# Optimization experiments

Measured on AMD Instinct MI355X. Metric: run time of the kernel, lower is better.

## Reference

```python
import jax, jax.numpy as jnp
import numpy as np

N, E = 20000, 160000
D_NODE_IN, D_EDGE_IN = 256, 64
D = 128          # node/edge feature dim
H = 256          # edge hidden dim
T = 17           # number of keypoint types
EDGE_STEPS, NODE_STEPS = 2, 1


def _w(k, shape):
    return jax.random.normal(k, shape, dtype=jnp.float32) / np.sqrt(shape[-2] if len(shape) > 1 else shape[-1]).astype(np.float32)


def setup_inputs() -> dict:
    key = jax.random.key(0)
    ks = iter(jax.random.split(key, 40))
    inp = {
        'x': jax.random.normal(next(ks), (N, D_NODE_IN), dtype=jnp.float32),
        'edge_attr': jax.random.normal(next(ks), (E, D_EDGE_IN), dtype=jnp.float32),
        'edge_index': jax.random.randint(next(ks), (2, E), 0, N),
        'node_types': jax.random.randint(next(ks), (N,), 0, T),
        # type-routed node embedding: 17 stacked 2-layer MLPs 256->128->128
        'ne_w1': _w(next(ks), (T, D_NODE_IN, D)), 'ne_b1': jnp.zeros((T, D)),
        'ne_w2': _w(next(ks), (T, D, D)),         'ne_b2': jnp.zeros((T, D)),
        # edge embedding 64->128->128
        'ee_w1': _w(next(ks), (D_EDGE_IN, D)), 'ee_b1': jnp.zeros((D,)),
        'ee_w2': _w(next(ks), (D, D)),         'ee_b2': jnp.zeros((D,)),
        # MPLayer edge MLP: [x_i, x_j, e] with skip -> (2*2D + 2D)=768 -> 256 -> 128
        'me_w1': _w(next(ks), (4 * D + 2 * D, H)), 'me_b1': jnp.zeros((H,)),
        'me_w2': _w(next(ks), (H, D)),             'me_b2': jnp.zeros((D,)),
        # MPLayer node update: [x(skip 2D), agg(D)] -> 128
        'mn_w1': _w(next(ks), (2 * D + D, D)), 'mn_b1': jnp.zeros((D,)),
        # classifiers
        'ec_w1': _w(next(ks), (D, D)), 'ec_b1': jnp.zeros((D,)),
        'ec_w2': _w(next(ks), (D, 1)), 'ec_b2': jnp.zeros((1,)),
        'nc_w1': _w(next(ks), (D, D)), 'nc_b1': jnp.zeros((D,)),
        'nc_w2': _w(next(ks), (D, 1)), 'nc_b2': jnp.zeros((1,)),
        'cc_w1': _w(next(ks), (D, D)), 'cc_b1': jnp.zeros((D,)),
        'cc_w2': _w(next(ks), (D, T)), 'cc_b2': jnp.zeros((T,)),
    }
    return inp


def _mlp2(x, w1, b1, w2, b2):
    return jax.nn.relu(x @ w1 + b1) @ w2 + b2


def reference(x, edge_attr, edge_index, node_types,
              ne_w1, ne_b1, ne_w2, ne_b2,
              ee_w1, ee_b1, ee_w2, ee_b2,
              me_w1, me_b1, me_w2, me_b2,
              mn_w1, mn_b1,
              ec_w1, ec_b1, ec_w2, ec_b2,
              nc_w1, nc_b1, nc_w2, nc_b2,
              cc_w1, cc_b1, cc_w2, cc_b2):
    n = x.shape[0]
    # NodeMlpType: run all 17 MLPs, select by node type (same math as masked dispatch)
    h = jax.nn.relu(jnp.einsum('nd,tdk->tnk', x, ne_w1) + ne_b1[:, None, :])   # [T,N,D]
    o = jnp.einsum('tnk,tkm->tnm', h, ne_w2) + ne_b2[:, None, :]               # [T,N,D]
    nf0 = o[node_types, jnp.arange(n)]                                          # [N,D]
    ef0 = _mlp2(edge_attr, ee_w1, ee_b1, ee_w2, ee_b2)                          # [E,D]

    src, dst = edge_index[0], edge_index[1]

    def mp_step(nf, ef):
        nf_c = jnp.concatenate([nf0, nf], axis=1)                               # skip concat [N,2D]
        ef_c = jnp.concatenate([ef0, ef], axis=1)                               # [E,2D]
        m = jnp.concatenate([nf_c[dst], nf_c[src], ef_c], axis=1)               # [E,6D]
        e_new = _mlp2(m, me_w1, me_b1, me_w2, me_b2)                            # [E,D]
        agg = jax.ops.segment_sum(e_new, dst, num_segments=n)                   # aggr='add'
        nf_new = jnp.concatenate([nf_c, agg], axis=1) @ mn_w1 + mn_b1           # [N,D]
        return nf_new, e_new

    nf, ef = nf0, ef0
    for _ in range(EDGE_STEPS):
        nf, ef = mp_step(nf, ef)
    pred_edge = _mlp2(ef, ec_w1, ec_b1, ec_w2, ec_b2).squeeze(-1)               # [E]
    for _ in range(NODE_STEPS):
        nf, ef = mp_step(nf, ef)
    pred_node = _mlp2(nf, nc_w1, nc_b1, nc_w2, nc_b2).squeeze(-1)               # [N]
    pred_class = _mlp2(nf, cc_w1, cc_b1, cc_w2, cc_b2)                          # [N,T]
    return (pred_edge, pred_node, pred_class, nf, ef)
```

## Files before the change

### kernel.cpp

```cpp
#include <hip/hip_runtime.h>
#include <hip/hip_bf16.h>

#define N_NODES 20000
#define N_EDGES 160000
#define DIN_NODE 256
#define DIN_EDGE 64
#define DF 128
#define HH 256
#define TT 17
#define NE_PAD_SLOTS 20544
#define NB_NODE (NE_PAD_SLOTS / 32)

typedef __attribute__((ext_vector_type(8))) short short8v;
typedef __attribute__((ext_vector_type(4))) float f32x4;

__device__ __forceinline__ unsigned short f2bf(float f) {
  unsigned int u = __builtin_bit_cast(unsigned int, f);
  u += 0x7FFFu + ((u >> 16) & 1u);
  return (unsigned short)(u >> 16);
}

__device__ __forceinline__ float bf2f(unsigned short u) {
  return __builtin_bit_cast(float, (unsigned int)u << 16);
}

__device__ __forceinline__ short8v pack8(float4 a, float4 b) {
  short8v o;
  o[0] = (short)f2bf(a.x); o[1] = (short)f2bf(a.y);
  o[2] = (short)f2bf(a.z); o[3] = (short)f2bf(a.w);
  o[4] = (short)f2bf(b.x); o[5] = (short)f2bf(b.y);
  o[6] = (short)f2bf(b.z); o[7] = (short)f2bf(b.w);
  return o;
}

struct PackPtrs {
  const float *s0, *s1, *s2, *s3, *s4, *s5, *s6, *s7, *s8, *s9, *s10, *s11;
  unsigned short *d0, *d1, *d2, *d3, *d4, *d5, *d6, *d7, *d8, *d9, *d10, *d11;
};

__global__ __launch_bounds__(256) void k_pack_all(PackPtrs P) {
  const int g = blockIdx.x * 4 + (threadIdx.x >> 6);
  const int l = threadIdx.x & 63;
  if (g >= 2320) return;
  const float* w; unsigned short* out; int K, N, tile;
  if (g < 128)       { w = P.s0;  out = P.d0;  K = 256; N = 256; tile = g; }
  else if (g < 256)  { w = P.s1;  out = P.d1;  K = 256; N = 256; tile = g - 128; }
  else if (g < 384)  { w = P.s2;  out = P.d2;  K = 256; N = 256; tile = g - 256; }
  else if (g < 448)  { w = P.s3;  out = P.d3;  K = 256; N = 128; tile = g - 384; }
  else if (g < 544)  { w = P.s4;  out = P.d4;  K = 384; N = 128; tile = g - 448; }
  else if (g < 1632) { w = P.s5;  out = P.d5;  K = 256; N = 128; tile = g - 544; }
  else if (g < 2176) { w = P.s6;  out = P.d6;  K = 128; N = 128; tile = g - 1632; }
  else if (g < 2192) { w = P.s7;  out = P.d7;  K = 64;  N = 128; tile = g - 2176; }
  else if (g < 2224) { w = P.s8;  out = P.d8;  K = 128; N = 128; tile = g - 2192; }
  else if (g < 2256) { w = P.s9;  out = P.d9;  K = 128; N = 128; tile = g - 2224; }
  else if (g < 2288) { w = P.s10; out = P.d10; K = 128; N = 128; tile = g - 2256; }
  else               { w = P.s11; out = P.d11; K = 128; N = 128; tile = g - 2288; }
  const int ntTiles = N >> 4;
  const int tilesPer = (K >> 5) * ntTiles;
  const int bt = tile / tilesPer;
  const int rr = tile - bt * tilesPer;
  const int kt = rr / ntTiles, nt = rr - kt * ntTiles;
  const float* wb = w + (size_t)bt * K * N;
  const int col = (nt << 4) + (l & 15);
  const int k0 = (kt << 5) + ((l >> 4) << 3);
  unsigned short* o = out + (((size_t)tile << 6) + l) * 8;
#pragma unroll
  for (int j = 0; j < 8; ++j) o[j] = f2bf(wb[(size_t)(k0 + j) * N + col]);
}

__global__ void k_count_deg(const int* __restrict__ types,
                            const int* __restrict__ dstv,
                            int* __restrict__ cnt, int* __restrict__ deg) {
  const int i = blockIdx.x * 256 + threadIdx.x;
  if (i < N_NODES) atomicAdd(&cnt[types[i]], 1);
  if (i < N_EDGES) atomicAdd(&deg[dstv[i]], 1);
}

__global__ __launch_bounds__(256) void k_prefix_scan(
    const int* __restrict__ cnt, int* __restrict__ woff,
    const int* __restrict__ deg, int* __restrict__ rs, int* __restrict__ wo) {
  __shared__ int partial[256];
  const int t = threadIdx.x;
  if (t == 0) {
    int cur = 0;
    for (int ty = 0; ty < TT; ++ty) {
      woff[ty] = cur;
      cur += (cnt[ty] + 31) & ~31;
    }
  }
  const int base = t * 80;
  int s = 0;
  for (int j = 0; j < 80; ++j) {
    const int n = base + j;
    if (n < N_NODES) s += deg[n];
  }
  partial[t] = s;
  __syncthreads();
  for (int off = 1; off < 256; off <<= 1) {
    const int v = (t >= off) ? partial[t - off] : 0;
    __syncthreads();
    partial[t] += v;
    __syncthreads();
  }
  int run = (t > 0) ? partial[t - 1] : 0;
  for (int j = 0; j < 80; ++j) {
    const int n = base + j;
    if (n < N_NODES) {
      rs[n] = run; wo[n] = run;
      run += deg[n];
    }
  }
  if (t == 255) rs[N_NODES] = run;
}

__global__ void k_scatter_elist(const int* __restrict__ types,
                                const int* __restrict__ srcv,
                                const int* __restrict__ dstv,
                                int* __restrict__ woff, int* __restrict__ wo,
                                int* __restrict__ bucket,
                                int* __restrict__ elist, int* __restrict__ ipos,
                                int* __restrict__ srcp, int* __restrict__ dstp) {
  const int i = blockIdx.x * 256 + threadIdx.x;
  if (i < N_NODES) {
    const int pos = atomicAdd(&woff[types[i]], 1);
    bucket[pos] = i;
  }
  if (i < N_EDGES) {
    const int pos = atomicAdd(&wo[dstv[i]], 1);
    elist[pos] = i;
    ipos[i] = pos;
    srcp[pos] = srcv[i];
    dstp[pos] = dstv[i];
  }
}

__global__ __launch_bounds__(256) void k_embed_fused(
    const float* __restrict__ x, const int* __restrict__ bucket,
    const int* __restrict__ types,
    const unsigned short* __restrict__ wp1, const float* __restrict__ b1,
    const unsigned short* __restrict__ wp2, const float* __restrict__ b2,
    unsigned short* __restrict__ nf0b,
    const unsigned short* __restrict__ wpd, const unsigned short* __restrict__ wps,
    unsigned short* __restrict__ PDo, unsigned short* __restrict__ PSo,
    const float* __restrict__ ea, const int* __restrict__ ipos,
    const unsigned short* __restrict__ ewp1, const float* __restrict__ eb1,
    const unsigned short* __restrict__ ewp2, const float* __restrict__ eb2,
    unsigned short* __restrict__ ef0p) {
  __shared__ __align__(16) unsigned char A[32 * 512];
  __shared__ __align__(16) unsigned char Hb[32 * 256];
  __shared__ int sidx[32];
  const int t = threadIdx.x;
  const int w = t >> 6, l = t & 63, lr = l & 15, lg = l >> 4;
  const int sw = (lr & 7) << 4;
  const int row0 = lr, row1 = 16 + lr;

  if (blockIdx.x < NB_NODE) {
    const int r0 = blockIdx.x * 32;
    if (t < 32) sidx[t] = bucket[r0 + t];
    __syncthreads();
    if (sidx[0] < 0) return;
    const int ty = types[sidx[0]];

#pragma unroll
    for (int j = 0; j < 4; ++j) {
      const int q = j * 256 + t;
      const int i = q >> 5, c = q & 31;
      const int nd = sidx[i];
      short8v o;
      if (nd >= 0) {
        const float* xr = x + (size_t)nd * DIN_NODE + c * 8;
        o = pack8(*reinterpret_cast<const float4*>(xr),
                  *reinterpret_cast<const float4*>(xr + 4));
      } else {
#pragma unroll
        for (int k = 0; k < 8; ++k) o[k] = 0;
      }
      *reinterpret_cast<short8v*>(A + ((i * 512 + c * 16) ^ ((i & 7) << 4))) = o;
    }
    __syncthreads();

    f32x4 acc[2][2];
#pragma unroll
    for (int mt = 0; mt < 2; ++mt)
#pragma unroll
      for (int q = 0; q < 2; ++q)
#pragma unroll
        for (int r = 0; r < 4; ++r) acc[mt][q][r] = 0.f;
#pragma unroll
    for (int kt = 0; kt < 8; ++kt) {
      const short8v a0 = *reinterpret_cast<const short8v*>(
          A + ((row0 * 512 + kt * 64 + lg * 16) ^ sw));
      const short8v a1 = *reinterpret_cast<const short8v*>(
          A + ((row1 * 512 + kt * 64 + lg * 16) ^ sw));
#pragma unroll
      for (int q = 0; q < 2; ++q) {
        const short8v bq = *reinterpret_cast<const short8v*>(
            wp1 + (((size_t)(ty * 64 + kt * 8 + 2 * w + q) * 64 + l) << 3));
        acc[0][q] = __builtin_amdgcn_mfma_f32_16x16x32_bf16(a0, bq, acc[0][q], 0, 0, 0);
        acc[1][q] = __builtin_amdgcn_mfma_f32_16x16x32_bf16(a1, bq, acc[1][q], 0, 0, 0);
      }
    }
#pragma unroll
    for (int q = 0; q < 2; ++q) {
      const int col = (2 * w + q) * 16 + lr;
      const float bias = b1[ty * DF + col];
#pragma unroll
      for (int mt = 0; mt < 2; ++mt)
#pragma unroll
        for (int r = 0; r < 4; ++r) {
          const int row = mt * 16 + lg * 4 + r;
          *reinterpret_cast<unsigned short*>(
              Hb + ((row * 256 + col * 2) ^ ((row & 7) << 4))) =
              f2bf(fmaxf(acc[mt][q][r] + bias, 0.f));
        }
    }
    __syncthreads();

    f32x4 acc2[2][2];
#pragma unroll
    for (int mt = 0; mt < 2; ++mt)
#pragma unroll
      for (int q = 0; q < 2; ++q)
#pragma unroll
        for (int r = 0; r < 4; ++r) acc2[mt][q][r] = 0.f;
#pragma unroll
    for (int kt = 0; kt < 4; ++kt) {
      const short8v a0 = *reinterpret_cast<const short8v*>(
          Hb + ((row0 * 256 + kt * 64 + lg * 16) ^ sw));
      const short8v a1 = *reinterpret_cast<const short8v*>(
          Hb + ((row1 * 256 + kt * 64 + lg * 16) ^ sw));
#pragma unroll
      for (int q = 0; q < 2; ++q) {
        const short8v bq = *reinterpret_cast<const short8v*>(
            wp2 + (((size_t)(ty * 32 + kt * 8 + 2 * w + q) * 64 + l) << 3));
        acc2[0][q] = __builtin_amdgcn_mfma_f32_16x16x32_bf16(a0, bq, acc2[0][q], 0, 0, 0);
        acc2[1][q] = __builtin_amdgcn_mfma_f32_16x16x32_bf16(a1, bq, acc2[1][q], 0, 0, 0);
      }
    }
#pragma unroll
    for (int q = 0; q < 2; ++q) {
      const int col = (2 * w + q) * 16 + lr;
      const float bias = b2[ty * DF + col];
#pragma unroll
      for (int mt = 0; mt < 2; ++mt)
#pragma unroll
        for (int r = 0; r < 4; ++r) {
          const int row = mt * 16 + lg * 4 + r;
          const int nd = sidx[row];
          const unsigned short v = f2bf(acc2[mt][q][r] + bias);
          if (nd >= 0) nf0b[(size_t)nd * DF + col] = v;
          *reinterpret_cast<unsigned short*>(
              A + ((row * 512 + col * 2) ^ ((row & 7) << 4))) = v;
          *reinterpret_cast<unsigned short*>(
              A + ((row * 512 + (col + 128) * 2) ^ ((row & 7) << 4))) = v;
        }
    }
    __syncthreads();

    f32x4 aD[2][4], aS[2][4];
#pragma unroll
    for (int mt = 0; mt < 2; ++mt)
#pragma unroll
      for (int q = 0; q < 4; ++q)
#pragma unroll
        for (int r = 0; r < 4; ++r) { aD[mt][q][r] = 0.f; aS[mt][q][r] = 0.f; }
    const int r0o = lr * 512 + lg * 16, r1o = (16 + lr) * 512 + lg * 16;
#pragma unroll
    for (int kt = 0; kt < 8; ++kt) {
      const short8v a0 = *reinterpret_cast<const short8v*>(A + ((r0o + kt * 64) ^ sw));
      const short8v a1 = *reinterpret_cast<const short8v*>(A + ((r1o + kt * 64) ^ sw));
#pragma unroll
      for (int q = 0; q < 4; ++q) {
        const size_t bi = (((size_t)(kt * 16 + 4 * w + q) * 64 + l) << 3);
        const short8v bD = *reinterpret_cast<const short8v*>(wpd + bi);
        const short8v bS = *reinterpret_cast<const short8v*>(wps + bi);
        aD[0][q] = __builtin_amdgcn_mfma_f32_16x16x32_bf16(a0, bD, aD[0][q], 0, 0, 0);
        aD[1][q] = __builtin_amdgcn_mfma_f32_16x16x32_bf16(a1, bD, aD[1][q], 0, 0, 0);
        aS[0][q] = __builtin_amdgcn_mfma_f32_16x16x32_bf16(a0, bS, aS[0][q], 0, 0, 0);
        aS[1][q] = __builtin_amdgcn_mfma_f32_16x16x32_bf16(a1, bS, aS[1][q], 0, 0, 0);
      }
    }
#pragma unroll
    for (int q = 0; q < 4; ++q) {
      const int col = (4 * w + q) * 16 + lr;
#pragma unroll
      for (int mt = 0; mt < 2; ++mt)
#pragma unroll
        for (int r = 0; r < 4; ++r) {
          const int row = mt * 16 + lg * 4 + r;
          const int nd = sidx[row];
          if (nd >= 0) {
            PDo[(size_t)nd * HH + col] = f2bf(aD[mt][q][r]);
            PSo[(size_t)nd * HH + col] = f2bf(aS[mt][q][r]);
          }
        }
    }
  } else {
    const int e0 = (blockIdx.x - NB_NODE) * 32;
    if (t < 32) sidx[t] = ipos[e0 + t];
    {
      const int i = t >> 3, c = t & 7;
      const float* xr = ea + (size_t)(e0 + i) * DIN_EDGE + c * 8;
      const short8v o = pack8(*reinterpret_cast<const float4*>(xr),
                              *reinterpret_cast<const float4*>(xr + 4));
      *reinterpret_cast<short8v*>(A + ((i * 128 + c * 16) ^ ((i & 7) << 4))) = o;
    }
    __syncthreads();

    f32x4 acc[2][2];
#pragma unroll
    for (int mt = 0; mt < 2; ++mt)
#pragma unroll
      for (int q = 0; q < 2; ++q)
#pragma unroll
        for (int r = 0; r < 4; ++r) acc[mt][q][r] = 0.f;
#pragma unroll
    for (int kt = 0; kt < 2; ++kt) {
      const short8v a0 = *reinterpret_cast<const short8v*>(
          A + ((row0 * 128 + kt * 64 + lg * 16) ^ sw));
      const short8v a1 = *reinterpret_cast<const short8v*>(
          A + ((row1 * 128 + kt * 64 + lg * 16) ^ sw));
#pragma unroll
      for (int q = 0; q < 2; ++q) {
        const short8v bq = *reinterpret_cast<const short8v*>(
            ewp1 + (((size_t)(kt * 8 + 2 * w + q) * 64 + l) << 3));
        acc[0][q] = __builtin_amdgcn_mfma_f32_16x16x32_bf16(a0, bq, acc[0][q], 0, 0, 0);
        acc[1][q] = __builtin_amdgcn_mfma_f32_16x16x32_bf16(a1, bq, acc[1][q], 0, 0, 0);
      }
    }
#pragma unroll
    for (int q = 0; q < 2; ++q) {
      const int col = (2 * w + q) * 16 + lr;
      const float bias = eb1[col];
#pragma unroll
      for (int mt = 0; mt < 2; ++mt)
#pragma unroll
        for (int r = 0; r < 4; ++r) {
          const int row = mt * 16 + lg * 4 + r;
          *reinterpret_cast<unsigned short*>(
              Hb + ((row * 256 + col * 2) ^ ((row & 7) << 4))) =
              f2bf(fmaxf(acc[mt][q][r] + bias, 0.f));
        }
    }
    __syncthreads();

    f32x4 acc2[2][2];
#pragma unroll
    for (int mt = 0; mt < 2; ++mt)
#pragma unroll
      for (int q = 0; q < 2; ++q)
#pragma unroll
        for (int r = 0; r < 4; ++r) acc2[mt][q][r] = 0.f;
#pragma unroll
    for (int kt = 0; kt < 4; ++kt) {
      const short8v a0 = *reinterpret_cast<const short8v*>(
          Hb + ((row0 * 256 + kt * 64 + lg * 16) ^ sw));
      const short8v a1 = *reinterpret_cast<const short8v*>(
          Hb + ((row1 * 256 + kt * 64 + lg * 16) ^ sw));
#pragma unroll
      for (int q = 0; q < 2; ++q) {
        const short8v bq = *reinterpret_cast<const short8v*>(
            ewp2 + (((size_t)(kt * 8 + 2 * w + q) * 64 + l) << 3));
        acc2[0][q] = __builtin_amdgcn_mfma_f32_16x16x32_bf16(a0, bq, acc2[0][q], 0, 0, 0);
        acc2[1][q] = __builtin_amdgcn_mfma_f32_16x16x32_bf16(a1, bq, acc2[1][q], 0, 0, 0);
      }
    }
#pragma unroll
    for (int q = 0; q < 2; ++q) {
      const int col = (2 * w + q) * 16 + lr;
      const float bias = eb2[col];
#pragma unroll
      for (int mt = 0; mt < 2; ++mt)
#pragma unroll
        for (int r = 0; r < 4; ++r) {
          const int row = mt * 16 + lg * 4 + r;
          ef0p[(size_t)sidx[row] * DF + col] = f2bf(acc2[mt][q][r] + bias);
        }
    }
  }
}

template <bool OUTF, bool HEAD>
__global__ __launch_bounds__(256) void k_edge_mlp_mfma(
    const unsigned short* __restrict__ ef0, const unsigned short* __restrict__ ef_in,
    unsigned short* __restrict__ ef_out, float* __restrict__ ef_outf,
    const int* __restrict__ srcp, const int* __restrict__ dstp,
    const int* __restrict__ elist,
    const unsigned short* __restrict__ wpe, const float* __restrict__ b1,
    const unsigned short* __restrict__ wp2, const float* __restrict__ b2,
    const unsigned short* __restrict__ PDi, const unsigned short* __restrict__ PSi,
    const unsigned short* __restrict__ wech, const float* __restrict__ hb1,
    const float* __restrict__ hw2, const float* __restrict__ hb2,
    float* __restrict__ out_pe) {
  __shared__ __align__(16) unsigned char A_lds[32 * 512];
  __shared__ __align__(16) unsigned char P_lds[32 * 512];
  __shared__ int sd[2][32];
  __shared__ int se[32];
  __shared__ float hpart[32][8];
  const int t = threadIdx.x;
  const int e0 = blockIdx.x * 32;
  if (t < 32) sd[0][t] = srcp[e0 + t];
  else if (t < 64) sd[1][t - 32] = dstp[e0 + t - 32];
  else if ((OUTF || HEAD) && t < 96) se[t - 64] = elist[e0 + t - 64];

#pragma unroll
  for (int j = 0; j < 4; ++j) {
    const int q = j * 256 + t;
    const int i = q >> 5, c = q & 31;
    const unsigned short* bp = (c < 16)
        ? ef0 + (size_t)(e0 + i) * DF + c * 8
        : ef_in + (size_t)(e0 + i) * DF + (c - 16) * 8;
    *reinterpret_cast<short8v*>(A_lds + ((i * 512 + c * 16) ^ ((i & 7) << 4))) =
        *reinterpret_cast<const short8v*>(bp);
  }
  __syncthreads();

#pragma unroll
  for (int j = 0; j < 4; ++j) {
    const int q = j * 256 + t;
    const int i = q >> 5, c = q & 31;
    const short8v pd = *reinterpret_cast<const short8v*>(
        PDi + (size_t)sd[1][i] * HH + c * 8);
    const short8v ps = *reinterpret_cast<const short8v*>(
        PSi + (size_t)sd[0][i] * HH + c * 8);
    short8v o;
#pragma unroll
    for (int k = 0; k < 8; ++k)
      o[k] = (short)f2bf(bf2f((unsigned short)pd[k]) + bf2f((unsigned short)ps[k]));
    *reinterpret_cast<short8v*>(P_lds + ((i * 512 + c * 16) ^ ((i & 7) << 4))) = o;
  }
  __syncthreads();

  const int w = t >> 6, l = t & 63, lr = l & 15, lg = l >> 4;
  const int swz = (lr & 7) << 4;

  f32x4 acc[2][4];
#pragma unroll
  for (int mt = 0; mt < 2; ++mt)
#pragma unroll
    for (int q = 0; q < 4; ++q) {
      const int col = (4 * w + q) * 16 + lr;
#pragma unroll
      for (int r = 0; r < 4; ++r) {
        const int row = mt * 16 + lg * 4 + r;
        const unsigned short u = *reinterpret_cast<const unsigned short*>(
            P_lds + ((row * 512 + col * 2) ^ ((row & 7) << 4)));
        acc[mt][q][r] = bf2f(u);
      }
    }

  const int r0o = lr * 512 + lg * 16;
  const int r1o = (16 + lr) * 512 + lg * 16;
  const unsigned short* wb1 = wpe + (((size_t)(4 * w) * 64 + l) << 3);

  short8v aR[3][2], bR[3][4];
#pragma unroll
  for (int s = 0; s < 2; ++s) {
    aR[s][0] = *reinterpret_cast<const short8v*>(A_lds + ((r0o + s * 64) ^ swz));
    aR[s][1] = *reinterpret_cast<const short8v*>(A_lds + ((r1o + s * 64) ^ swz));
#pragma unroll
    for (int q = 0; q < 4; ++q)
      bR[s][q] = *reinterpret_cast<const short8v*>(wb1 + (size_t)s * 8192 + q * 512);
  }
#pragma unroll
  for (int kt = 0; kt < 8; ++kt) {
    const int cur = kt % 3, pf = (kt + 2) % 3;
    if (kt < 6) {
      aR[pf][0] = *reinterpret_cast<const short8v*>(
          A_lds + ((r0o + (kt + 2) * 64) ^ swz));
      aR[pf][1] = *reinterpret_cast<const short8v*>(
          A_lds + ((r1o + (kt + 2) * 64) ^ swz));
#pragma unroll
      for (int q = 0; q < 4; ++q)
        bR[pf][q] = *reinterpret_cast<const short8v*>(
            wb1 + (size_t)(kt + 2) * 8192 + q * 512);
    }
#pragma unroll
    for (int q = 0; q < 4; ++q) {
      acc[0][q] = __builtin_amdgcn_mfma_f32_16x16x32_bf16(aR[cur][0], bR[cur][q],
                                                          acc[0][q], 0, 0, 0);
      acc[1][q] = __builtin_amdgcn_mfma_f32_16x16x32_bf16(aR[cur][1], bR[cur][q],
                                                          acc[1][q], 0, 0, 0);
    }
  }
  __syncthreads();

#pragma unroll
  for (int q = 0; q < 4; ++q) {
    const int col = (4 * w + q) * 16 + lr;
    const float bias = b1[col];
#pragma unroll
    for (int mt = 0; mt < 2; ++mt)
#pragma unroll
      for (int r = 0; r < 4; ++r) {
        const int row = mt * 16 + lg * 4 + r;
        *reinterpret_cast<unsigned short*>(
            P_lds + ((row * 512 + col * 2) ^ ((row & 7) << 4))) =
            f2bf(fmaxf(acc[mt][q][r] + bias, 0.f));
      }
  }
  __syncthreads();

  f32x4 acc2[2][2];
#pragma unroll
  for (int mt = 0; mt < 2; ++mt)
#pragma unroll
    for (int q = 0; q < 2; ++q)
#pragma unroll
      for (int r = 0; r < 4; ++r) acc2[mt][q][r] = 0.f;

  const int h0o = lr * 512 + lg * 16;
  const int h1o = (16 + lr) * 512 + lg * 16;
  const unsigned short* wb2 = wp2 + (((size_t)(2 * w) * 64 + l) << 3);

  short8v aS[3][2], bS[3][2];
#pragma unroll
  for (int s = 0; s < 2; ++s) {
    aS[s][0] = *reinterpret_cast<const short8v*>(P_lds + ((h0o + s * 64) ^ swz));
    aS[s][1] = *reinterpret_cast<const short8v*>(P_lds + ((h1o + s * 64) ^ swz));
#pragma unroll
    for (int q = 0; q < 2; ++q)
      bS[s][q] = *reinterpret_cast<const short8v*>(wb2 + (size_t)s * 4096 + q * 512);
  }
#pragma unroll
  for (int kt = 0; kt < 8; ++kt) {
    const int cur = kt % 3, pf = (kt + 2) % 3;
    if (kt < 6) {
      aS[pf][0] = *reinterpret_cast<const short8v*>(
          P_lds + ((h0o + (kt + 2) * 64) ^ swz));
      aS[pf][1] = *reinterpret_cast<const short8v*>(
          P_lds + ((h1o + (kt + 2) * 64) ^ swz));
#pragma unroll
      for (int q = 0; q < 2; ++q)
        bS[pf][q] = *reinterpret_cast<const short8v*>(
            wb2 + (size_t)(kt + 2) * 4096 + q * 512);
    }
#pragma unroll
    for (int q = 0; q < 2; ++q) {
      acc2[0][q] = __builtin_amdgcn_mfma_f32_16x16x32_bf16(aS[cur][0], bS[cur][q],
                                                           acc2[0][q], 0, 0, 0);
      acc2[1][q] = __builtin_amdgcn_mfma_f32_16x16x32_bf16(aS[cur][1], bS[cur][q],
                                                           acc2[1][q], 0, 0, 0);
    }
  }

#pragma unroll
  for (int q = 0; q < 2; ++q) {
    const int n = (2 * w + q) * 16 + lr;
    const float bias = b2[n];
#pragma unroll
    for (int mt = 0; mt < 2; ++mt)
#pragma unroll
      for (int r = 0; r < 4; ++r) {
        const int m = mt * 16 + lg * 4 + r;
        const float v = acc2[mt][q][r] + bias;
        ef_out[(size_t)(e0 + m) * DF + n] = f2bf(v);
        if (OUTF)
          ef_outf[(size_t)se[m] * DF + n] = v;
      }
  }

  if constexpr (HEAD) {
    __syncthreads();
#pragma unroll
    for (int q = 0; q < 2; ++q) {
      const int n = (2 * w + q) * 16 + lr;
      const float bias = b2[n];
#pragma unroll
      for (int mt = 0; mt < 2; ++mt)
#pragma unroll
        for (int r = 0; r < 4; ++r) {
          const int m = mt * 16 + lg * 4 + r;
          *reinterpret_cast<unsigned short*>(
              P_lds + ((m * 256 + n * 2) ^ ((m & 7) << 4))) =
              f2bf(acc2[mt][q][r] + bias);
        }
    }
    __syncthreads();
    f32x4 ah[2][2];
#pragma unroll
    for (int mt = 0; mt < 2; ++mt)
#pragma unroll
      for (int q = 0; q < 2; ++q)
#pragma unroll
        for (int r = 0; r < 4; ++r) ah[mt][q][r] = 0.f;
#pragma unroll
    for (int kt = 0; kt < 4; ++kt) {
      const short8v a0 = *reinterpret_cast<const short8v*>(
          P_lds + ((lr * 256 + kt * 64 + lg * 16) ^ swz));
      const short8v a1 = *reinterpret_cast<const short8v*>(
          P_lds + (((16 + lr) * 256 + kt * 64 + lg * 16) ^ swz));
#pragma unroll
      for (int q = 0; q < 2; ++q) {
        const short8v bq = *reinterpret_cast<const short8v*>(
            wech + (((size_t)(kt * 8 + 2 * w + q) * 64 + l) << 3));
        ah[0][q] = __builtin_amdgcn_mfma_f32_16x16x32_bf16(a0, bq, ah[0][q], 0, 0, 0);
        ah[1][q] = __builtin_amdgcn_mfma_f32_16x16x32_bf16(a1, bq, ah[1][q], 0, 0, 0);
      }
    }
#pragma unroll
    for (int q = 0; q < 2; ++q) {
      const int col = (2 * w + q) * 16 + lr;
      const float bias = hb1[col];
#pragma unroll
      for (int mt = 0; mt < 2; ++mt)
#pragma unroll
        for (int r = 0; r < 4; ++r) {
          const int row = mt * 16 + lg * 4 + r;
          *reinterpret_cast<unsigned short*>(A_lds + row * 256 + col * 2) =
              f2bf(fmaxf(ah[mt][q][r] + bias, 0.f));
        }
    }
    __syncthreads();
    {
      const int rr = t >> 3, kc = t & 7;
      float s = 0.f;
#pragma unroll
      for (int u = 0; u < 16; ++u)
        s = fmaf(bf2f(*reinterpret_cast<const unsigned short*>(
                     A_lds + rr * 256 + (kc * 16 + u) * 2)),
                 hw2[kc * 16 + u], s);
      hpart[rr][kc] = s;
    }
    __syncthreads();
    if (t < 32) {
      float s = hb2[0];
#pragma unroll
      for (int k = 0; k < 8; ++k) s += hpart[t][k];
      out_pe[se[t]] = s;
    }
  }
}

template <bool OUTF, bool PART>
__global__ __launch_bounds__(256) void k_node_update_mfma(
    const unsigned short* __restrict__ nf0, const unsigned short* __restrict__ nfb,
    const unsigned short* __restrict__ efp,
    const int* __restrict__ rs, void* __restrict__ outp,
    const unsigned short* __restrict__ wp, const float* __restrict__ b,
    const unsigned short* __restrict__ wpd, const unsigned short* __restrict__ wps,
    unsigned short* __restrict__ PDo, unsigned short* __restrict__ PSo) {
  __shared__ __align__(16) unsigned char A[32 * 768];
  const int t = threadIdx.x;
  const int n0 = blockIdx.x * 32;
#pragma unroll
  for (int j = 0; j < 4; ++j) {
    const int q = j * 256 + t;
    const int i = q >> 5, c = q & 31;
    const unsigned short* bp = (c < 16)
        ? nf0 + (size_t)(n0 + i) * DF + c * 8
        : nfb + (size_t)(n0 + i) * DF + (c - 16) * 8;
    *reinterpret_cast<short8v*>(A + ((i * 768 + c * 16) ^ ((i & 7) << 4))) =
        *reinterpret_cast<const short8v*>(bp);
  }
  {
    const int i = t >> 3, sub = t & 7;
    const int n = n0 + i;
    const int kb = rs[n], ke = rs[n + 1];
    float av[16];
#pragma unroll
    for (int u = 0; u < 16; ++u) av[u] = 0.f;
    for (int k = kb; k < ke; ++k) {
      const unsigned short* er = efp + (size_t)k * DF + sub * 16;
      const short8v v0 = *reinterpret_cast<const short8v*>(er);
      const short8v v1 = *reinterpret_cast<const short8v*>(er + 8);
#pragma unroll
      for (int u = 0; u < 8; ++u) {
        av[u] += bf2f((unsigned short)v0[u]);
        av[8 + u] += bf2f((unsigned short)v1[u]);
      }
    }
    short8v o0, o1;
#pragma unroll
    for (int u = 0; u < 8; ++u) {
      o0[u] = (short)f2bf(av[u]);
      o1[u] = (short)f2bf(av[8 + u]);
    }
    const int c0 = 32 + sub * 2;
    *reinterpret_cast<short8v*>(A + ((i * 768 + c0 * 16) ^ ((i & 7) << 4))) = o0;
    *reinterpret_cast<short8v*>(A + ((i * 768 + (c0 + 1) * 16) ^ ((i & 7) << 4))) = o1;
  }
  __syncthreads();

  const int w = t >> 6, l = t & 63, lr = l & 15, lg = l >> 4;
  const int sw = (lr & 7) << 4;
  const int row0 = lr, row1 = 16 + lr;

  f32x4 acc[2][2];
#pragma unroll
  for (int mt = 0; mt < 2; ++mt)
#pragma unroll
    for (int q = 0; q < 2; ++q)
#pragma unroll
      for (int r = 0; r < 4; ++r) acc[mt][q][r] = 0.f;
#pragma unroll
  for (int kt = 0; kt < 12; ++kt) {
    const short8v a0 = *reinterpret_cast<const short8v*>(
        A + ((row0 * 768 + kt * 64 + lg * 16) ^ sw));
    const short8v a1 = *reinterpret_cast<const short8v*>(
        A + ((row1 * 768 + kt * 64 + lg * 16) ^ sw));
#pragma unroll
    for (int q = 0; q < 2; ++q) {
      const short8v bq = *reinterpret_cast<const short8v*>(
          wp + (((size_t)(kt * 8 + 2 * w + q) * 64 + l) << 3));
      acc[0][q] = __builtin_amdgcn_mfma_f32_16x16x32_bf16(a0, bq, acc[0][q], 0, 0, 0);
      acc[1][q] = __builtin_amdgcn_mfma_f32_16x16x32_bf16(a1, bq, acc[1][q], 0, 0, 0);
    }
  }
#pragma unroll
  for (int q = 0; q < 2; ++q) {
    const int col = (2 * w + q) * 16 + lr;
    const float bias = b[col];
#pragma unroll
    for (int mt = 0; mt < 2; ++mt)
#pragma unroll
      for (int r = 0; r < 4; ++r) {
        const int row = mt * 16 + lg * 4 + r;
        const float v = acc[mt][q][r] + bias;
        if (OUTF)
          ((float*)outp)[(size_t)(n0 + row) * DF + col] = v;
        else
          ((unsigned short*)outp)[(size_t)(n0 + row) * DF + col] = f2bf(v);
      }
  }

  if constexpr (PART) {
    __syncthreads();
#pragma unroll
    for (int q = 0; q < 2; ++q) {
      const int col = (2 * w + q) * 16 + lr;
      const float bias = b[col];
#pragma unroll
      for (int mt = 0; mt < 2; ++mt)
#pragma unroll
        for (int r = 0; r < 4; ++r) {
          const int row = mt * 16 + lg * 4 + r;
          *reinterpret_cast<unsigned short*>(
              A + ((row * 768 + 256 + col * 2) ^ ((row & 7) << 4))) =
              f2bf(acc[mt][q][r] + bias);
        }
    }
    __syncthreads();
    f32x4 aD[2][4], aSv[2][4];
#pragma unroll
    for (int mt = 0; mt < 2; ++mt)
#pragma unroll
      for (int q = 0; q < 4; ++q)
#pragma unroll
        for (int r = 0; r < 4; ++r) { aD[mt][q][r] = 0.f; aSv[mt][q][r] = 0.f; }
    const int r0p = lr * 768 + lg * 16, r1p = (16 + lr) * 768 + lg * 16;
#pragma unroll
    for (int kt = 0; kt < 8; ++kt) {
      const short8v a0 = *reinterpret_cast<const short8v*>(A + ((r0p + kt * 64) ^ sw));
      const short8v a1 = *reinterpret_cast<const short8v*>(A + ((r1p + kt * 64) ^ sw));
#pragma unroll
      for (int q = 0; q < 4; ++q) {
        const size_t bi = (((size_t)(kt * 16 + 4 * w + q) * 64 + l) << 3);
        const short8v bD = *reinterpret_cast<const short8v*>(wpd + bi);
        const short8v bSv = *reinterpret_cast<const short8v*>(wps + bi);
        aD[0][q] = __builtin_amdgcn_mfma_f32_16x16x32_bf16(a0, bD, aD[0][q], 0, 0, 0);
        aD[1][q] = __builtin_amdgcn_mfma_f32_16x16x32_bf16(a1, bD, aD[1][q], 0, 0, 0);
        aSv[0][q] = __builtin_amdgcn_mfma_f32_16x16x32_bf16(a0, bSv, aSv[0][q], 0, 0, 0);
        aSv[1][q] = __builtin_amdgcn_mfma_f32_16x16x32_bf16(a1, bSv, aSv[1][q], 0, 0, 0);
      }
    }
#pragma unroll
    for (int q = 0; q < 4; ++q) {
      const int col = (4 * w + q) * 16 + lr;
#pragma unroll
      for (int mt = 0; mt < 2; ++mt)
#pragma unroll
        for (int r = 0; r < 4; ++r) {
          const int row = mt * 16 + lg * 4 + r;
          PDo[(size_t)(n0 + row) * HH + col] = f2bf(aD[mt][q][r]);
          PSo[(size_t)(n0 + row) * HH + col] = f2bf(aSv[mt][q][r]);
        }
    }
  }
}

template <bool INBF>
__global__ __launch_bounds__(256) void k_cls_scalar_mfma(
    const void* __restrict__ feat, const unsigned short* __restrict__ wp,
    const float* __restrict__ b1, const float* __restrict__ w2,
    const float* __restrict__ b2, float* __restrict__ out) {
  __shared__ __align__(16) unsigned char A[32 * 256];
  __shared__ float hid[32][136];
  __shared__ float w2s[DF];
  __shared__ float part[32][8];
  const int t = threadIdx.x;
  const int r0 = blockIdx.x * 32;
  if (t < DF) w2s[t] = w2[t];
#pragma unroll
  for (int j = 0; j < 2; ++j) {
    const int q = j * 256 + t;
    const int i = q >> 4, c = q & 15;
    short8v o;
    if (INBF) {
      o = *reinterpret_cast<const short8v*>(
          (const unsigned short*)feat + (size_t)(r0 + i) * DF + c * 8);
    } else {
      const float* fr = (const float*)feat + (size_t)(r0 + i) * DF + c * 8;
      o = pack8(*reinterpret_cast<const float4*>(fr),
                *reinterpret_cast<const float4*>(fr + 4));
    }
    *reinterpret_cast<short8v*>(A + ((i * 256 + c * 16) ^ ((i & 7) << 4))) = o;
  }
  __syncthreads();

  const int w = t >> 6, l = t & 63, lr = l & 15, lg = l >> 4;
  const int sw = (lr & 7) << 4;
  const int row0 = lr, row1 = 16 + lr;
  f32x4 acc[2][2];
#pragma unroll
  for (int mt = 0; mt < 2; ++mt)
#pragma unroll
    for (int q = 0; q < 2; ++q)
#pragma unroll
      for (int r = 0; r < 4; ++r) acc[mt][q][r] = 0.f;
#pragma unroll
  for (int kt = 0; kt < 4; ++kt) {
    const short8v a0 = *reinterpret_cast<const short8v*>(
        A + ((row0 * 256 + kt * 64 + lg * 16) ^ sw));
    const short8v a1 = *reinterpret_cast<const short8v*>(
        A + ((row1 * 256 + kt * 64 + lg * 16) ^ sw));
#pragma unroll
    for (int q = 0; q < 2; ++q) {
      const short8v bq = *reinterpret_cast<const short8v*>(
          wp + (((size_t)(kt * 8 + 2 * w + q) * 64 + l) << 3));
      acc[0][q] = __builtin_amdgcn_mfma_f32_16x16x32_bf16(a0, bq, acc[0][q], 0, 0, 0);
      acc[1][q] = __builtin_amdgcn_mfma_f32_16x16x32_bf16(a1, bq, acc[1][q], 0, 0, 0);
    }
  }
#pragma unroll
  for (int q = 0; q < 2; ++q) {
    const int col = (2 * w + q) * 16 + lr;
    const float bias = b1[col];
#pragma unroll
    for (int mt = 0; mt < 2; ++mt)
#pragma unroll
      for (int r = 0; r < 4; ++r) {
        const int row = mt * 16 + lg * 4 + r;
        hid[row][col] = fmaxf(acc[mt][q][r] + bias, 0.f);
      }
  }
  __syncthreads();
  {
    const int r = t >> 3, kc = t & 7;
    float s = 0.f;
#pragma unroll
    for (int u = 0; u < 16; ++u) s = fmaf(hid[r][kc * 16 + u], w2s[kc * 16 + u], s);
    part[r][kc] = s;
  }
  __syncthreads();
  if (t < 32) {
    float s = b2[0];
#pragma unroll
    for (int k = 0; k < 8; ++k) s += part[t][k];
    out[r0 + t] = s;
  }
}

__global__ __launch_bounds__(256) void k_cls_class_mfma(
    const float* __restrict__ feat, const unsigned short* __restrict__ wp,
    const float* __restrict__ b1, const float* __restrict__ w2,
    const float* __restrict__ b2, float* __restrict__ out) {
  __shared__ __align__(16) unsigned char A[32 * 256];
  __shared__ float hid[32][136];
  __shared__ float w2s[DF * TT];
  const int t = threadIdx.x;
  const int r0 = blockIdx.x * 32;
  for (int j = t; j < DF * TT; j += 256) w2s[j] = w2[j];
#pragma unroll
  for (int j = 0; j < 2; ++j) {
    const int q = j * 256 + t;
    const int i = q >> 4, c = q & 15;
    const float* fr = feat + (size_t)(r0 + i) * DF + c * 8;
    const short8v o = pack8(*reinterpret_cast<const float4*>(fr),
                            *reinterpret_cast<const float4*>(fr + 4));
    *reinterpret_cast<short8v*>(A + ((i * 256 + c * 16) ^ ((i & 7) << 4))) = o;
  }
  __syncthreads();

  const int w = t >> 6, l = t & 63, lr = l & 15, lg = l >> 4;
  const int sw = (lr & 7) << 4;
  const int row0 = lr, row1 = 16 + lr;
  f32x4 acc[2][2];
#pragma unroll
  for (int mt = 0; mt < 2; ++mt)
#pragma unroll
    for (int q = 0; q < 2; ++q)
#pragma unroll
      for (int r = 0; r < 4; ++r) acc[mt][q][r] = 0.f;
#pragma unroll
  for (int kt = 0; kt < 4; ++kt) {
    const short8v a0 = *reinterpret_cast<const short8v*>(
        A + ((row0 * 256 + kt * 64 + lg * 16) ^ sw));
    const short8v a1 = *reinterpret_cast<const short8v*>(
        A + ((row1 * 256 + kt * 64 + lg * 16) ^ sw));
#pragma unroll
    for (int q = 0; q < 2; ++q) {
      const short8v bq = *reinterpret_cast<const short8v*>(
          wp + (((size_t)(kt * 8 + 2 * w + q) * 64 + l) << 3));
      acc[0][q] = __builtin_amdgcn_mfma_f32_16x16x32_bf16(a0, bq, acc[0][q], 0, 0, 0);
      acc[1][q] = __builtin_amdgcn_mfma_f32_16x16x32_bf16(a1, bq, acc[1][q], 0, 0, 0);
    }
  }
#pragma unroll
  for (int q = 0; q < 2; ++q) {
    const int col = (2 * w + q) * 16 + lr;
    const float bias = b1[col];
#pragma unroll
    for (int mt = 0; mt < 2; ++mt)
#pragma unroll
      for (int r = 0; r < 4; ++r) {
        const int row = mt * 16 + lg * 4 + r;
        hid[row][col] = fmaxf(acc[mt][q][r] + bias, 0.f);
      }
  }
  __syncthreads();
  for (int o = t; o < 32 * TT; o += 256) {
    const int r = o / TT, c = o - TT * r;
    float s = b2[c];
    for (int k = 0; k < DF; ++k) s = fmaf(hid[r][k], w2s[k * TT + c], s);
    out[(size_t)(r0 + r) * TT + c] = s;
  }
}

extern "C" void kernel_launch(void* const* d_in, const int* in_sizes, int n_in,
                              void* d_out, int out_size, void* d_ws,
                              size_t ws_size, hipStream_t stream) {
  (void)in_sizes; (void)n_in; (void)out_size; (void)ws_size;
  const float* x         = (const float*)d_in[0];
  const float* edge_attr = (const float*)d_in[1];
  const int*   edge_idx  = (const int*)d_in[2];
  const int*   node_ty   = (const int*)d_in[3];
  const float* ne_w1 = (const float*)d_in[4];
  const float* ne_b1 = (const float*)d_in[5];
  const float* ne_w2 = (const float*)d_in[6];
  const float* ne_b2 = (const float*)d_in[7];
  const float* ee_w1 = (const float*)d_in[8];
  const float* ee_b1 = (const float*)d_in[9];
  const float* ee_w2 = (const float*)d_in[10];
  const float* ee_b2 = (const float*)d_in[11];
  const float* me_w1 = (const float*)d_in[12];
  const float* me_b1 = (const float*)d_in[13];
  const float* me_w2 = (const float*)d_in[14];
  const float* me_b2 = (const float*)d_in[15];
  const float* mn_w1 = (const float*)d_in[16];
  const float* mn_b1 = (const float*)d_in[17];
  const float* ec_w1 = (const float*)d_in[18];
  const float* ec_b1 = (const float*)d_in[19];
  const float* ec_w2 = (const float*)d_in[20];
  const float* ec_b2 = (const float*)d_in[21];
  const float* nc_w1 = (const float*)d_in[22];
  const float* nc_b1 = (const float*)d_in[23];
  const float* nc_w2 = (const float*)d_in[24];
  const float* nc_b2 = (const float*)d_in[25];
  const float* cc_w1 = (const float*)d_in[26];
  const float* cc_b1 = (const float*)d_in[27];
  const float* cc_w2 = (const float*)d_in[28];
  const float* cc_b2 = (const float*)d_in[29];

  const int* srcv = edge_idx;
  const int* dstv = edge_idx + N_EDGES;

  unsigned short* nf0b = (unsigned short*)d_ws;
  unsigned short* nf1b = nf0b + (size_t)N_NODES * DF;
  unsigned short* ef0p = nf1b + (size_t)N_NODES * DF;
  unsigned short* ef1p = ef0p + (size_t)N_EDGES * DF;
  unsigned short* wmpD = ef1p + (size_t)N_EDGES * DF;
  unsigned short* wmpS = wmpD + 256 * 256;
  unsigned short* wmeE = wmpS + 256 * 256;
  unsigned short* wme2 = wmeE + 256 * 256;
  unsigned short* wmn  = wme2 + 256 * 128;
  unsigned short* wne1 = wmn + 384 * 128;
  unsigned short* wne2 = wne1 + (size_t)TT * 256 * 128;
  unsigned short* wee1 = wne2 + (size_t)TT * 128 * 128;
  unsigned short* wee2 = wee1 + 64 * 128;
  unsigned short* wec  = wee2 + 128 * 128;
  unsigned short* wnc  = wec + 128 * 128;
  unsigned short* wcc  = wnc + 128 * 128;
  unsigned short* PD   = wcc + 128 * 128;
  unsigned short* PS   = PD + (size_t)N_NODES * HH;
  int* cnt    = (int*)(PS + (size_t)N_NODES * HH);
  int* woff   = cnt + 32;
  int* bucket = woff + 32;
  int* deg    = bucket + NE_PAD_SLOTS;
  int* rs     = deg + N_NODES;
  int* wo     = rs + N_NODES + 1;
  int* elist  = wo + N_NODES;
  int* ipos   = elist + N_EDGES;
  int* srcp   = ipos + N_EDGES;
  int* dstp   = srcp + N_EDGES;

  float* out_pe = (float*)d_out;
  float* out_pn = out_pe + N_EDGES;
  float* out_pc = out_pn + N_NODES;
  float* out_nf = out_pc + (size_t)N_NODES * TT;
  float* out_ef = out_nf + (size_t)N_NODES * DF;

  PackPtrs P;
  P.s0 = me_w1;            P.d0 = wmpD;
  P.s1 = me_w1 + 256*256;  P.d1 = wmpS;
  P.s2 = me_w1 + 512*256;  P.d2 = wmeE;
  P.s3 = me_w2;            P.d3 = wme2;
  P.s4 = mn_w1;            P.d4 = wmn;
  P.s5 = ne_w1;            P.d5 = wne1;
  P.s6 = ne_w2;            P.d6 = wne2;
  P.s7 = ee_w1;            P.d7 = wee1;
  P.s8 = ee_w2;            P.d8 = wee2;
  P.s9 = ec_w1;            P.d9 = wec;
  P.s10 = nc_w1;           P.d10 = wnc;
  P.s11 = cc_w1;           P.d11 = wcc;
  k_pack_all<<<580, 256, 0, stream>>>(P);

  hipMemsetAsync(cnt, 0, 32 * sizeof(int), stream);
  hipMemsetAsync(deg, 0, N_NODES * sizeof(int), stream);
  hipMemsetAsync(bucket, 0xFF, NE_PAD_SLOTS * sizeof(int), stream);
  k_count_deg<<<(N_EDGES + 255) / 256, 256, 0, stream>>>(node_ty, dstv, cnt, deg);
  k_prefix_scan<<<1, 256, 0, stream>>>(cnt, woff, deg, rs, wo);
  k_scatter_elist<<<(N_EDGES + 255) / 256, 256, 0, stream>>>(
      node_ty, srcv, dstv, woff, wo, bucket, elist, ipos, srcp, dstp);

  k_embed_fused<<<NB_NODE + N_EDGES / 32, 256, 0, stream>>>(
      x, bucket, node_ty, wne1, ne_b1, wne2, ne_b2, nf0b, wmpD, wmpS, PD, PS,
      edge_attr, ipos, wee1, ee_b1, wee2, ee_b2, ef0p);

  k_edge_mlp_mfma<false, false><<<N_EDGES / 32, 256, 0, stream>>>(
      ef0p, ef0p, ef1p, nullptr, srcp, dstp, elist, wmeE, me_b1, wme2, me_b2,
      PD, PS, nullptr, nullptr, nullptr, nullptr, nullptr);
  k_node_update_mfma<false, true><<<N_NODES / 32, 256, 0, stream>>>(
      nf0b, nf0b, ef1p, rs, (void*)nf1b, wmn, mn_b1, wmpD, wmpS, PD, PS);
  k_edge_mlp_mfma<false, true><<<N_EDGES / 32, 256, 0, stream>>>(
      ef0p, ef1p, ef1p, nullptr, srcp, dstp, elist, wmeE, me_b1, wme2, me_b2,
      PD, PS, wec, ec_b1, ec_w2, ec_b2, out_pe);
  k_node_update_mfma<false, true><<<N_NODES / 32, 256, 0, stream>>>(
      nf0b, nf1b, ef1p, rs, (void*)nf1b, wmn, mn_b1, wmpD, wmpS, PD, PS);
  k_edge_mlp_mfma<true, false><<<N_EDGES / 32, 256, 0, stream>>>(
      ef0p, ef1p, ef1p, out_ef, srcp, dstp, elist, wmeE, me_b1, wme2, me_b2,
      PD, PS, nullptr, nullptr, nullptr, nullptr, nullptr);
  k_node_update_mfma<true, false><<<N_NODES / 32, 256, 0, stream>>>(
      nf0b, nf1b, ef1p, rs, (void*)out_nf, wmn, mn_b1, wmpD, wmpS, PD, PS);

  k_cls_scalar_mfma<false><<<N_NODES / 32, 256, 0, stream>>>(
      (const void*)out_nf, wnc, nc_b1, nc_w2, nc_b2, out_pn);
  k_cls_class_mfma<<<N_NODES / 32, 256, 0, stream>>>(out_nf, wcc, cc_b1, cc_w2,
                                                     cc_b2, out_pc);
}
```

Measured before the change: 575.3 us.

## Batch gather loads in edge MLP and fuse two node classifier kernels

The edge MLP kernel now loads src/dst indices directly and issues all feature and PD/PS gather loads into registers before any LDS writes, so one barrier is dropped and more memory requests are in flight. It also adds an occupancy hint of 4 blocks per CU. The two node classifier kernels are merged into one that reads node features once and computes both heads from the shared LDS tile, saving a launch and one feature read. The trade-off is higher register pressure in the edge kernel under the launch-bounds cap, which could cause spills.

```diff
diff --git a/kernel.cpp b/kernel.cpp
--- a/kernel.cpp
+++ b/kernel.cpp
@@ -381,7 +381,7 @@
 }
 
 template <bool OUTF, bool HEAD>
-__global__ __launch_bounds__(256) void k_edge_mlp_mfma(
+__global__ __launch_bounds__(256, 4) void k_edge_mlp_mfma(
     const unsigned short* __restrict__ ef0, const unsigned short* __restrict__ ef_in,
     unsigned short* __restrict__ ef_out, float* __restrict__ ef_outf,
     const int* __restrict__ srcp, const int* __restrict__ dstp,
@@ -394,15 +394,13 @@
     float* __restrict__ out_pe) {
   __shared__ __align__(16) unsigned char A_lds[32 * 512];
   __shared__ __align__(16) unsigned char P_lds[32 * 512];
-  __shared__ int sd[2][32];
   __shared__ int se[32];
   __shared__ float hpart[32][8];
   const int t = threadIdx.x;
   const int e0 = blockIdx.x * 32;
-  if (t < 32) sd[0][t] = srcp[e0 + t];
-  else if (t < 64) sd[1][t - 32] = dstp[e0 + t - 32];
-  else if ((OUTF || HEAD) && t < 96) se[t - 64] = elist[e0 + t - 64];
-
+  if ((OUTF || HEAD) && t < 32) se[t] = elist[e0 + t];
+
+  short8v av[4], pdv[4], psv[4];
 #pragma unroll
   for (int j = 0; j < 4; ++j) {
     const int q = j * 256 + t;
@@ -410,24 +408,29 @@
     const unsigned short* bp = (c < 16)
         ? ef0 + (size_t)(e0 + i) * DF + c * 8
         : ef_in + (size_t)(e0 + i) * DF + (c - 16) * 8;
-    *reinterpret_cast<short8v*>(A_lds + ((i * 512 + c * 16) ^ ((i & 7) << 4))) =
-        *reinterpret_cast<const short8v*>(bp);
-  }
-  __syncthreads();
-
+    av[j] = *reinterpret_cast<const short8v*>(bp);
+  }
 #pragma unroll
   for (int j = 0; j < 4; ++j) {
     const int q = j * 256 + t;
     const int i = q >> 5, c = q & 31;
-    const short8v pd = *reinterpret_cast<const short8v*>(
-        PDi + (size_t)sd[1][i] * HH + c * 8);
-    const short8v ps = *reinterpret_cast<const short8v*>(
-        PSi + (size_t)sd[0][i] * HH + c * 8);
+    const int dn = dstp[e0 + i];
+    const int sn = srcp[e0 + i];
+    pdv[j] = *reinterpret_cast<const short8v*>(PDi + (size_t)dn * HH + c * 8);
+    psv[j] = *reinterpret_cast<const short8v*>(PSi + (size_t)sn * HH + c * 8);
+  }
+#pragma unroll
+  for (int j = 0; j < 4; ++j) {
+    const int q = j * 256 + t;
+    const int i = q >> 5, c = q & 31;
+    const int off = (i * 512 + c * 16) ^ ((i & 7) << 4);
+    *reinterpret_cast<short8v*>(A_lds + off) = av[j];
     short8v o;
 #pragma unroll
     for (int k = 0; k < 8; ++k)
-      o[k] = (short)f2bf(bf2f((unsigned short)pd[k]) + bf2f((unsigned short)ps[k]));
-    *reinterpret_cast<short8v*>(P_lds + ((i * 512 + c * 16) ^ ((i & 7) << 4))) = o;
+      o[k] = (short)f2bf(bf2f((unsigned short)pdv[j][k]) +
+                         bf2f((unsigned short)psv[j][k]));
+    *reinterpret_cast<short8v*>(P_lds + off) = o;
   }
   __syncthreads();
 
@@ -779,98 +782,22 @@
   }
 }
 
-template <bool INBF>
-__global__ __launch_bounds__(256) void k_cls_scalar_mfma(
-    const void* __restrict__ feat, const unsigned short* __restrict__ wp,
-    const float* __restrict__ b1, const float* __restrict__ w2,
-    const float* __restrict__ b2, float* __restrict__ out) {
+__global__ __launch_bounds__(256) void k_cls_both_mfma(
+    const float* __restrict__ feat,
+    const unsigned short* __restrict__ wpn, const float* __restrict__ nb1,
+    const float* __restrict__ nw2, const float* __restrict__ nb2,
+    const unsigned short* __restrict__ wpc, const float* __restrict__ cb1,
+    const float* __restrict__ cw2, const float* __restrict__ cb2,
+    float* __restrict__ out_pn, float* __restrict__ out_pc) {
   __shared__ __align__(16) unsigned char A[32 * 256];
   __shared__ float hid[32][136];
-  __shared__ float w2s[DF];
+  __shared__ float w2s[DF * TT];
+  __shared__ float nw2s[DF];
   __shared__ float part[32][8];
   const int t = threadIdx.x;
   const int r0 = blockIdx.x * 32;
-  if (t < DF) w2s[t] = w2[t];
-#pragma unroll
-  for (int j = 0; j < 2; ++j) {
-    const int q = j * 256 + t;
-    const int i = q >> 4, c = q & 15;
-    short8v o;
-    if (INBF) {
-      o = *reinterpret_cast<const short8v*>(
-          (const unsigned short*)feat + (size_t)(r0 + i) * DF + c * 8);
-    } else {
-      const float* fr = (const float*)feat + (size_t)(r0 + i) * DF + c * 8;
-      o = pack8(*reinterpret_cast<const float4*>(fr),
-                *reinterpret_cast<const float4*>(fr + 4));
-    }
-    *reinterpret_cast<short8v*>(A + ((i * 256 + c * 16) ^ ((i & 7) << 4))) = o;
-  }
-  __syncthreads();
-
-  const int w = t >> 6, l = t & 63, lr = l & 15, lg = l >> 4;
-  const int sw = (lr & 7) << 4;
-  const int row0 = lr, row1 = 16 + lr;
-  f32x4 acc[2][2];
-#pragma unroll
-  for (int mt = 0; mt < 2; ++mt)
-#pragma unroll
-    for (int q = 0; q < 2; ++q)
-#pragma unroll
-      for (int r = 0; r < 4; ++r) acc[mt][q][r] = 0.f;
-#pragma unroll
-  for (int kt = 0; kt < 4; ++kt) {
-    const short8v a0 = *reinterpret_cast<const short8v*>(
-        A + ((row0 * 256 + kt * 64 + lg * 16) ^ sw));
-    const short8v a1 = *reinterpret_cast<const short8v*>(
-        A + ((row1 * 256 + kt * 64 + lg * 16) ^ sw));
-#pragma unroll
-    for (int q = 0; q < 2; ++q) {
-      const short8v bq = *reinterpret_cast<const short8v*>(
-          wp + (((size_t)(kt * 8 + 2 * w + q) * 64 + l) << 3));
-      acc[0][q] = __builtin_amdgcn_mfma_f32_16x16x32_bf16(a0, bq, acc[0][q], 0, 0, 0);
-      acc[1][q] = __builtin_amdgcn_mfma_f32_16x16x32_bf16(a1, bq, acc[1][q], 0, 0, 0);
-    }
-  }
-#pragma unroll
-  for (int q = 0; q < 2; ++q) {
-    const int col = (2 * w + q) * 16 + lr;
-    const float bias = b1[col];
-#pragma unroll
-    for (int mt = 0; mt < 2; ++mt)
-#pragma unroll
-      for (int r = 0; r < 4; ++r) {
-        const int row = mt * 16 + lg * 4 + r;
-        hid[row][col] = fmaxf(acc[mt][q][r] + bias, 0.f);
-      }
-  }
-  __syncthreads();
-  {
-    const int r = t >> 3, kc = t & 7;
-    float s = 0.f;
-#pragma unroll
-    for (int u = 0; u < 16; ++u) s = fmaf(hid[r][kc * 16 + u], w2s[kc * 16 + u], s);
-    part[r][kc] = s;
-  }
-  __syncthreads();
-  if (t < 32) {
-    float s = b2[0];
-#pragma unroll
-    for (int k = 0; k < 8; ++k) s += part[t][k];
-    out[r0 + t] = s;
-  }
-}
-
-__global__ __launch_bounds__(256) void k_cls_class_mfma(
-    const float* __restrict__ feat, const unsigned short* __restrict__ wp,
-    const float* __restrict__ b1, const float* __restrict__ w2,
-    const float* __restrict__ b2, float* __restrict__ out) {
-  __shared__ __align__(16) unsigned char A[32 * 256];
-  __shared__ float hid[32][136];
-  __shared__ float w2s[DF * TT];
-  const int t = threadIdx.x;
-  const int r0 = blockIdx.x * 32;
-  for (int j = t; j < DF * TT; j += 256) w2s[j] = w2[j];
+  for (int j = t; j < DF * TT; j += 256) w2s[j] = cw2[j];
+  if (t < DF) nw2s[t] = nw2[t];
 #pragma unroll
   for (int j = 0; j < 2; ++j) {
     const int q = j * 256 + t;
@@ -885,6 +812,7 @@
   const int w = t >> 6, l = t & 63, lr = l & 15, lg = l >> 4;
   const int sw = (lr & 7) << 4;
   const int row0 = lr, row1 = 16 + lr;
+
   f32x4 acc[2][2];
 #pragma unroll
   for (int mt = 0; mt < 2; ++mt)
@@ -901,7 +829,7 @@
 #pragma unroll
     for (int q = 0; q < 2; ++q) {
       const short8v bq = *reinterpret_cast<const short8v*>(
-          wp + (((size_t)(kt * 8 + 2 * w + q) * 64 + l) << 3));
+          wpn + (((size_t)(kt * 8 + 2 * w + q) * 64 + l) << 3));
       acc[0][q] = __builtin_amdgcn_mfma_f32_16x16x32_bf16(a0, bq, acc[0][q], 0, 0, 0);
       acc[1][q] = __builtin_amdgcn_mfma_f32_16x16x32_bf16(a1, bq, acc[1][q], 0, 0, 0);
     }
@@ -909,7 +837,7 @@
 #pragma unroll
   for (int q = 0; q < 2; ++q) {
     const int col = (2 * w + q) * 16 + lr;
-    const float bias = b1[col];
+    const float bias = nb1[col];
 #pragma unroll
     for (int mt = 0; mt < 2; ++mt)
 #pragma unroll
@@ -919,11 +847,61 @@
       }
   }
   __syncthreads();
+  {
+    const int r = t >> 3, kc = t & 7;
+    float s = 0.f;
+#pragma unroll
+    for (int u = 0; u < 16; ++u) s = fmaf(hid[r][kc * 16 + u], nw2s[kc * 16 + u], s);
+    part[r][kc] = s;
+  }
+  __syncthreads();
+  if (t < 32) {
+    float s = nb2[0];
+#pragma unroll
+    for (int k = 0; k < 8; ++k) s += part[t][k];
+    out_pn[r0 + t] = s;
+  }
+  __syncthreads();
+
+  f32x4 acc2[2][2];
+#pragma unroll
+  for (int mt = 0; mt < 2; ++mt)
+#pragma unroll
+    for (int q = 0; q < 2; ++q)
+#pragma unroll
+      for (int r = 0; r < 4; ++r) acc2[mt][q][r] = 0.f;
+#pragma unroll
+  for (int kt = 0; kt < 4; ++kt) {
+    const short8v a0 = *reinterpret_cast<const short8v*>(
+        A + ((row0 * 256 + kt * 64 + lg * 16) ^ sw));
+    const short8v a1 = *reinterpret_cast<const short8v*>(
+        A + ((row1 * 256 + kt * 64 + lg * 16) ^ sw));
+#pragma unroll
+    for (int q = 0; q < 2; ++q) {
+      const short8v bq = *reinterpret_cast<const short8v*>(
+          wpc + (((size_t)(kt * 8 + 2 * w + q) * 64 + l) << 3));
+      acc2[0][q] = __builtin_amdgcn_mfma_f32_16x16x32_bf16(a0, bq, acc2[0][q], 0, 0, 0);
+      acc2[1][q] = __builtin_amdgcn_mfma_f32_16x16x32_bf16(a1, bq, acc2[1][q], 0, 0, 0);
+    }
+  }
+#pragma unroll
+  for (int q = 0; q < 2; ++q) {
+    const int col = (2 * w + q) * 16 + lr;
+    const float bias = cb1[col];
+#pragma unroll
+    for (int mt = 0; mt < 2; ++mt)
+#pragma unroll
+      for (int r = 0; r < 4; ++r) {
+        const int row = mt * 16 + lg * 4 + r;
+        hid[row][col] = fmaxf(acc2[mt][q][r] + bias, 0.f);
+      }
+  }
+  __syncthreads();
   for (int o = t; o < 32 * TT; o += 256) {
     const int r = o / TT, c = o - TT * r;
-    float s = b2[c];
+    float s = cb2[c];
     for (int k = 0; k < DF; ++k) s = fmaf(hid[r][k], w2s[k * TT + c], s);
-    out[(size_t)(r0 + r) * TT + c] = s;
+    out_pc[(size_t)(r0 + r) * TT + c] = s;
   }
 }
 
@@ -1043,8 +1021,7 @@
   k_node_update_mfma<true, false><<<N_NODES / 32, 256, 0, stream>>>(
       nf0b, nf1b, ef1p, rs, (void*)out_nf, wmn, mn_b1, wmpD, wmpS, PD, PS);
 
-  k_cls_scalar_mfma<false><<<N_NODES / 32, 256, 0, stream>>>(
-      (const void*)out_nf, wnc, nc_b1, nc_w2, nc_b2, out_pn);
-  k_cls_class_mfma<<<N_NODES / 32, 256, 0, stream>>>(out_nf, wcc, cc_b1, cc_w2,
-                                                     cc_b2, out_pc);
-}
+  k_cls_both_mfma<<<N_NODES / 32, 256, 0, stream>>>(
+      out_nf, wnc, nc_b1, nc_w2, nc_b2, wcc, cc_b1, cc_w2, cc_b2, out_pn,
+      out_pc);
+}
```

Result: faster. 554.5 us (-3.6%).
